# Kernel tuning notes

Measured on AMD Instinct MI355X. Metric: run time of the kernel, lower is better.

The kernel has to match this reference:

```python
import jax, jax.numpy as jnp
import numpy as np
import math

HEADS = 16
MAX_LEN = 512  # tokens; seq must equal this for the relative bias to be valid
D_HEAD = 64
BH = 256  # batch*heads


def setup_inputs() -> dict:
    key = jax.random.key(0)
    k1, k2, k3, k4 = jax.random.split(key, 4)
    S, B, D = MAX_LEN, BH, D_HEAD
    return {
        "query": jax.random.normal(k1, (S, B, D), dtype=jnp.float32),
        "key": jax.random.normal(k2, (S, B, D), dtype=jnp.float32),
        "value": jax.random.normal(k3, (S, B, D), dtype=jnp.float32),
        # per-head relative position embedding table [heads, 2*tokens-1, d_head]
        "k_rpos_emb": jax.random.normal(k4, (HEADS, 2 * MAX_LEN - 1, D), dtype=jnp.float32),
    }


def reference(query, key, value, k_rpos_emb):
    # 'seq b f -> b seq f'
    q = jnp.transpose(query, (1, 0, 2))   # [bh, s, d]
    k = jnp.transpose(key, (1, 0, 2))
    v = jnp.transpose(value, (1, 0, 2))
    bh, s, d = q.shape
    b = bh // HEADS

    # relative position bias from keys: split heads, contract with per-head table
    kh = k.reshape(b, HEADS, s, d)                                   # [b,h,s,d]
    rel_logits = jnp.einsum('bhid,hrd->bhir', kh, k_rpos_emb)        # [b,h,s,2L-1]
    rel_idx = (jnp.arange(s)[None, :] - jnp.arange(s)[:, None]
               + MAX_LEN - 1).astype(jnp.int32)                      # [s,s] in [0,2L-2]
    rel_bias = jnp.take_along_axis(
        rel_logits, rel_idx[None, None, :, :], axis=-1)              # [b,h,s,s]
    rel_bias = rel_bias.reshape(bh, s, s)

    scale = 1.0 / math.sqrt(d)
    scores = (jnp.einsum('bid,bjd->bij', q, k) + rel_bias) * scale   # [bh,s,s]
    attn = jax.nn.softmax(scores, axis=-1)
    out = jnp.einsum('bij,bjd->bid', attn, v)                        # [bh,s,d]
    return jnp.transpose(out, (1, 0, 2))                             # [s,bh,d]
```

## Files before the change

kernel.cpp:

```cpp
#include <hip/hip_runtime.h>
#include <hip/hip_bf16.h>

#define S_LEN  512
#define D_DIM  64
#define NH     16
#define R_LEN  1023
#define BHD    16384
#define PPITCH 68

typedef __attribute__((ext_vector_type(8))) short   short8_t;
typedef __attribute__((ext_vector_type(8))) __bf16  bf16x8;
typedef __attribute__((ext_vector_type(4))) float   floatx4;

__device__ __forceinline__ unsigned short f2bf(float f) {
  union { float f; unsigned u; } v; v.f = f;
  return (unsigned short)((v.u + 0x7fffu + ((v.u >> 16) & 1u)) >> 16);
}
__device__ __forceinline__ ushort2 c2(float x, float y) {
  __hip_bfloat162 h = __float22bfloat162_rn(float2{x, y});
  union { __hip_bfloat162 h; ushort2 u; } v; v.h = h; return v.u;
}
__device__ __forceinline__ short8_t pack8s(float4 a, float4 b) {
  union { ushort2 u2[4]; short8_t s8; } u;
  u.u2[0] = c2(a.x, a.y); u.u2[1] = c2(a.z, a.w);
  u.u2[2] = c2(b.x, b.y); u.u2[3] = c2(b.z, b.w);
  return u.s8;
}
__device__ __forceinline__ bf16x8 pack8(float4 a, float4 b) {
  short8_t s = pack8s(a, b);
  return __builtin_bit_cast(bf16x8, s);
}
__device__ __forceinline__ bf16x8 ldfrag(const unsigned short* p) {
  short8_t s = *(const short8_t*)p;
  return __builtin_bit_cast(bf16x8, s);
}
__device__ __forceinline__ bf16x8 ldfrag8(const unsigned short* p) {
  union { ushort4 u4[2]; short8_t s8; } u;
  u.u4[0] = *(const ushort4*)p;
  u.u4[1] = *(const ushort4*)(p + 4);
  return __builtin_bit_cast(bf16x8, u.s8);
}
__device__ __forceinline__ bf16x8 ldseg(const unsigned short* buf, int r, int seg) {
  return ldfrag(buf + r * 64 + ((seg ^ (r & 7)) << 3));
}
__device__ __forceinline__ void async16(const void* g, void* l) {
  __builtin_amdgcn_global_load_lds(
      (const __attribute__((address_space(1))) unsigned int*)(unsigned long long)(uintptr_t)g,
      (__attribute__((address_space(3))) unsigned int*)(unsigned int)(uintptr_t)l,
      16, 0, 0);
}
__device__ __forceinline__ void stage16(const unsigned short* gb, size_t rstride,
                                        unsigned short* lb, int lane) {
  int srow = lane >> 3;
  int sseg = (lane & 7) ^ srow;
  async16(gb + (size_t)srow * rstride + sseg * 8, lb);
  async16(gb + (size_t)(srow + 8) * rstride + sseg * 8, lb + 512);
}
__device__ __forceinline__ void stageE(const unsigned short* gb, int sigma,
                                       unsigned short* slot, int lane, int wv) {
  int srow = lane >> 3;
  int sseg = (lane & 7) ^ srow;
  int r0 = sigma * 64 + wv * 16 + srow;
  unsigned short* lb = slot + (wv * 16) * 64;
  async16(gb + (size_t)min(r0, R_LEN - 1) * D_DIM + sseg * 8, lb);
  async16(gb + (size_t)min(r0 + 8, R_LEN - 1) * D_DIM + sseg * 8, lb + 512);
}
template<int N>
__device__ __forceinline__ float dpp_ror(float x) {
  int i = __builtin_bit_cast(int, x);
  int r = __builtin_amdgcn_update_dpp(i, i, 0x120 + N, 0xF, 0xF, false);
  return __builtin_bit_cast(float, r);
}
__device__ __forceinline__ float rmax16(float x) {
  x = fmaxf(x, dpp_ror<8>(x)); x = fmaxf(x, dpp_ror<4>(x));
  x = fmaxf(x, dpp_ror<2>(x)); x = fmaxf(x, dpp_ror<1>(x));
  return x;
}
__device__ __forceinline__ float rsum16(float x) {
  x += dpp_ror<8>(x); x += dpp_ror<4>(x);
  x += dpp_ror<2>(x); x += dpp_ror<1>(x);
  return x;
}

extern "C" __global__ void prepass(const float* __restrict__ k, const float* __restrict__ v,
                                   const float* __restrict__ emb,
                                   unsigned short* __restrict__ kb,
                                   unsigned short* __restrict__ vtb,
                                   unsigned short* __restrict__ eb) {
  __shared__ unsigned short t[64 * PPITCH];
  const int bid = blockIdx.x;
  const int tid = threadIdx.x;
  if (bid < 4096) {
    size_t i = (size_t)bid * 256 + tid;
    const float* s = k + i * 8;
    float4 a = *(const float4*)s, b = *(const float4*)(s + 4);
    *(short8_t*)(kb + i * 8) = pack8s(a, b);
  } else if (bid < 4608) {
    size_t i = (size_t)(bid - 4096) * 256 + tid;
    if (i < 130944) {
      const float* s = emb + i * 8;
      float4 a = *(const float4*)s, b = *(const float4*)(s + 4);
      *(short8_t*)(eb + i * 8) = pack8s(a, b);
    }
  } else {
    const int b2 = bid - 4608;
    const int bh = b2 >> 3;
    const int j0 = (b2 & 7) << 6;
    for (int idx = tid; idx < 1024; idx += 256) {
      int jl = idx >> 4, cg = (idx & 15) << 2;
      float4 a = *(const float4*)(v + (size_t)(j0 + jl) * BHD + bh * D_DIM + cg);
      ushort2 u0 = c2(a.x, a.y), u1 = c2(a.z, a.w);
      *(ushort4*)(t + jl * PPITCH + cg) = (ushort4){ u0.x, u0.y, u1.x, u1.y };
    }
    __syncthreads();
    for (int slot = tid; slot < 512; slot += 256) {
      int d = slot >> 3, jseg = slot & 7;
      union { unsigned short u[8]; short8_t s8; } r;
      #pragma unroll
      for (int jj = 0; jj < 8; ++jj) r.u[jj] = t[(jseg * 8 + jj) * PPITCH + d];
      *(short8_t*)(vtb + ((size_t)bh * D_DIM + d) * S_LEN + j0 + jseg * 8) = r.s8;
    }
  }
}

extern "C" __global__ __launch_bounds__(256, 2)
void attn_relbias(const float* __restrict__ q, const unsigned short* __restrict__ kb,
                  const unsigned short* __restrict__ vtb,
                  const unsigned short* __restrict__ eb,
                  float* __restrict__ out)
{
  __shared__ unsigned short kbuf[2][4096];
  __shared__ unsigned short vbuf[2][4096];
  __shared__ unsigned short ebuf[3][4096];
  __shared__ unsigned short ps[4][16 * PPITCH];

  const int tid  = threadIdx.x;
  const int bh   = blockIdx.x & 255;
  const int i0   = (blockIdx.x >> 8) << 6;
  const int h    = bh & (NH - 1);
  const int wv   = tid >> 6;
  const int lane = tid & 63;
  const int l15  = lane & 15;
  const int quad = lane >> 4;
  const int iloc0 = wv * 16 + quad * 4;
  const int elo   = 3 - wv;
  const int arow  = wv * 16 + l15;
  const int acol  = quad * 8;
  const int it0   = 7 - (i0 >> 6);

  const unsigned short* kgb  = kb  + (size_t)bh * D_DIM;
  const unsigned short* vgb  = vtb + (size_t)bh * (D_DIM * S_LEN);
  const unsigned short* egb  = eb  + (size_t)h * (R_LEN * D_DIM);

  stage16(kgb + (size_t)(wv * 16) * BHD, BHD, &kbuf[0][(wv * 16) * 64], lane);
  stage16(vgb + (size_t)(wv * 16) * S_LEN, S_LEN, &vbuf[0][(wv * 16) * 64], lane);
  stageE(egb, it0,     ebuf[it0 % 3],       lane, wv);
  stageE(egb, it0 + 1, ebuf[(it0 + 1) % 3], lane, wv);

  bf16x8 qa0, qa1, ia0, ia1;
  {
    const float* gq = q + (size_t)(i0 + arow) * BHD + bh * D_DIM + acol;
    qa0 = pack8(*(const float4*)gq,        *(const float4*)(gq + 4));
    qa1 = pack8(*(const float4*)(gq + 32), *(const float4*)(gq + 36));
    const unsigned short* gi = kb + (size_t)(i0 + arow) * BHD + bh * D_DIM + acol;
    ia0 = ldfrag(gi);
    ia1 = ldfrag(gi + 32);
  }

  floatx4 oacc[4];
  #pragma unroll
  for (int c = 0; c < 4; ++c) oacc[c] = (floatx4){0.f, 0.f, 0.f, 0.f};
  float m_i[4] = { -1e30f, -1e30f, -1e30f, -1e30f };
  float l_i[4] = { 0.f, 0.f, 0.f, 0.f };

  __syncthreads();

  #pragma unroll 2
  for (int t = 0; t < 8; ++t) {
    if (t < 7) {
      const int j1 = t * 64 + 64;
      stage16(kgb + (size_t)(j1 + wv * 16) * BHD, BHD, &kbuf[(t + 1) & 1][(wv * 16) * 64], lane);
      stage16(vgb + (size_t)(wv * 16) * S_LEN + j1, S_LEN, &vbuf[(t + 1) & 1][(wv * 16) * 64], lane);
      stageE(egb, it0 + t + 2, ebuf[(it0 + t + 2) % 3], lane, wv);
    }
    const unsigned short* kc = kbuf[t & 1];
    const unsigned short* vc = vbuf[t & 1];

    floatx4 bacc[5];
    #pragma unroll
    for (int ei = 0; ei < 5; ++ei) {
      const int eblk = elo + ei;
      const unsigned short* es = ebuf[(it0 + t + (eblk >> 2)) % 3];
      const int lr = (eblk * 16 + l15) & 63;
      floatx4 bz = (floatx4){0.f, 0.f, 0.f, 0.f};
      bz = __builtin_amdgcn_mfma_f32_16x16x32_bf16(ia0, ldseg(es, lr, quad),     bz, 0, 0, 0);
      bz = __builtin_amdgcn_mfma_f32_16x16x32_bf16(ia1, ldseg(es, lr, quad + 4), bz, 0, 0, 0);
      bacc[ei] = bz;
    }

    floatx4 qk[4];
    #pragma unroll
    for (int c = 0; c < 4; ++c) {
      floatx4 acc = (floatx4){0.f, 0.f, 0.f, 0.f};
      acc = __builtin_amdgcn_mfma_f32_16x16x32_bf16(qa0, ldseg(kc, c * 16 + l15, quad),     acc, 0, 0, 0);
      acc = __builtin_amdgcn_mfma_f32_16x16x32_bf16(qa1, ldseg(kc, c * 16 + l15, quad + 4), acc, 0, 0, 0);
      qk[c] = acc;
    }

    float sc[4][4];
    #pragma unroll
    for (int r = 0; r < 4; ++r) {
      const int o  = 15 - 4 * quad - r;
      const int ls = (lane & 48) + ((l15 + o) & 15);
      const bool hi = (l15 + o) >= 16;
      #pragma unroll
      for (int c = 0; c < 4; ++c) {
        float blo = __shfl(bacc[c][r],     ls);
        float bhi = __shfl(bacc[c + 1][r], ls);
        sc[c][r] = (qk[c][r] + (hi ? bhi : blo)) * 0.125f;
      }
    }

    float p[4][4];
    #pragma unroll
    for (int r = 0; r < 4; ++r) {
      float mx = fmaxf(fmaxf(sc[0][r], sc[1][r]), fmaxf(sc[2][r], sc[3][r]));
      mx = rmax16(mx);
      float mnew  = fmaxf(m_i[r], mx);
      float alpha = __expf(m_i[r] - mnew);
      float rs = 0.f;
      #pragma unroll
      for (int c = 0; c < 4; ++c) { p[c][r] = __expf(sc[c][r] - mnew); rs += p[c][r]; }
      rs = rsum16(rs);
      l_i[r] = l_i[r] * alpha + rs;
      m_i[r] = mnew;
      #pragma unroll
      for (int c = 0; c < 4; ++c) oacc[c][r] *= alpha;
    }

    unsigned short* psw = ps[wv];
    #pragma unroll
    for (int r = 0; r < 4; ++r) {
      ushort2 u01 = c2(p[0][r], p[1][r]);
      ushort2 u23 = c2(p[2][r], p[3][r]);
      unsigned short* pr = psw + (quad * 4 + r) * PPITCH + l15;
      pr[0]  = u01.x; pr[16] = u01.y; pr[32] = u23.x; pr[48] = u23.y;
    }
    bf16x8 pa0 = ldfrag8(psw + l15 * PPITCH + acol);
    bf16x8 pa1 = ldfrag8(psw + l15 * PPITCH + acol + 32);

    #pragma unroll
    for (int c = 0; c < 4; ++c) {
      oacc[c] = __builtin_amdgcn_mfma_f32_16x16x32_bf16(pa0, ldseg(vc, c * 16 + l15, quad),     oacc[c], 0, 0, 0);
      oacc[c] = __builtin_amdgcn_mfma_f32_16x16x32_bf16(pa1, ldseg(vc, c * 16 + l15, quad + 4), oacc[c], 0, 0, 0);
    }

    __syncthreads();
  }

  #pragma unroll
  for (int r = 0; r < 4; ++r) {
    float inv = 1.f / l_i[r];
    int row = i0 + iloc0 + r;
    #pragma unroll
    for (int c = 0; c < 4; ++c)
      out[(size_t)row * BHD + bh * D_DIM + c * 16 + l15] = oacc[c][r] * inv;
  }
}

#define PITCH 72
extern "C" __global__ __launch_bounds__(256, 4)
void attn_fb(const float* __restrict__ q, const float* __restrict__ k,
             const float* __restrict__ v, const float* __restrict__ emb,
             float* __restrict__ out)
{
  __shared__ unsigned short kjs[64 * PITCH];
  __shared__ unsigned short vts[64 * PITCH];
  __shared__ unsigned short ps2[4][16 * PPITCH];

  const int tid  = threadIdx.x;
  const int bh   = blockIdx.x >> 3;
  const int i0   = (blockIdx.x & 7) << 6;
  const int h    = bh & (NH - 1);
  const int wv   = tid >> 6;
  const int lane = tid & 63;
  const int l15  = lane & 15;
  const int quad = lane >> 4;
  const int iloc0 = wv * 16 + quad * 4;
  const int elo   = 3 - wv;

  {
    const float* gq = q + (size_t)i0 * BHD + bh * D_DIM;
    const float* gk = k + (size_t)i0 * BHD + bh * D_DIM;
    for (int idx = tid; idx < 1024; idx += 256) {
      int row = idx >> 4, cg = (idx & 15) << 2;
      float4 a = *(const float4*)(gq + row * BHD + cg);
      float4 b = *(const float4*)(gk + row * BHD + cg);
      *(ushort4*)(vts + row * PITCH + cg) = (ushort4){ f2bf(a.x), f2bf(a.y), f2bf(a.z), f2bf(a.w) };
      *(ushort4*)(kjs + row * PITCH + cg) = (ushort4){ f2bf(b.x), f2bf(b.y), f2bf(b.z), f2bf(b.w) };
    }
  }
  __syncthreads();

  const int arow = wv * 16 + l15;
  const int acol = quad * 8;
  bf16x8 qa0 = ldfrag(vts + arow * PITCH + acol);
  bf16x8 qa1 = ldfrag(vts + arow * PITCH + acol + 32);
  bf16x8 ia0 = ldfrag(kjs + arow * PITCH + acol);
  bf16x8 ia1 = ldfrag(kjs + arow * PITCH + acol + 32);

  floatx4 oacc[4];
  #pragma unroll
  for (int c = 0; c < 4; ++c) oacc[c] = (floatx4){0.f, 0.f, 0.f, 0.f};
  float m_i[4] = { -1e30f, -1e30f, -1e30f, -1e30f };
  float l_i[4] = { 0.f, 0.f, 0.f, 0.f };

  for (int j0 = 0; j0 < S_LEN; j0 += 64) {
    __syncthreads();
    {
      const float* gk = k + (size_t)j0 * BHD + bh * D_DIM;
      for (int idx = tid; idx < 1024; idx += 256) {
        int row = idx >> 4, cg = (idx & 15) << 2;
        float4 b = *(const float4*)(gk + row * BHD + cg);
        *(ushort4*)(kjs + row * PITCH + cg) = (ushort4){ f2bf(b.x), f2bf(b.y), f2bf(b.z), f2bf(b.w) };
      }
    }
    {
      const float* gv = v + (size_t)j0 * BHD + bh * D_DIM;
      for (int idx = tid; idx < 1024; idx += 256) {
        int dg = idx & 15, jl = idx >> 4;
        float4 b = *(const float4*)(gv + jl * BHD + dg * 4);
        int d0 = dg * 4;
        vts[(d0 + 0) * PITCH + jl] = f2bf(b.x);
        vts[(d0 + 1) * PITCH + jl] = f2bf(b.y);
        vts[(d0 + 2) * PITCH + jl] = f2bf(b.z);
        vts[(d0 + 3) * PITCH + jl] = f2bf(b.w);
      }
    }
    floatx4 bacc[5];
    {
      const int rbase = j0 - i0 + 448;
      #pragma unroll
      for (int ei = 0; ei < 5; ++ei) {
        int rg = rbase + (elo + ei) * 16 + l15;
        rg = min(rg, R_LEN - 1);
        const float* ep = emb + ((size_t)h * R_LEN + rg) * D_DIM + acol;
        float4 e0 = *(const float4*)(ep);
        float4 e1 = *(const float4*)(ep + 4);
        float4 e2 = *(const float4*)(ep + 32);
        float4 e3 = *(const float4*)(ep + 36);
        floatx4 bz = (floatx4){0.f, 0.f, 0.f, 0.f};
        bz = __builtin_amdgcn_mfma_f32_16x16x32_bf16(ia0, pack8(e0, e1), bz, 0, 0, 0);
        bz = __builtin_amdgcn_mfma_f32_16x16x32_bf16(ia1, pack8(e2, e3), bz, 0, 0, 0);
        bacc[ei] = bz;
      }
    }
    __syncthreads();

    floatx4 qk[4];
    #pragma unroll
    for (int c = 0; c < 4; ++c) {
      bf16x8 kb0 = ldfrag(kjs + (c * 16 + l15) * PITCH + acol);
      bf16x8 kb1 = ldfrag(kjs + (c * 16 + l15) * PITCH + acol + 32);
      floatx4 acc = (floatx4){0.f, 0.f, 0.f, 0.f};
      acc = __builtin_amdgcn_mfma_f32_16x16x32_bf16(qa0, kb0, acc, 0, 0, 0);
      acc = __builtin_amdgcn_mfma_f32_16x16x32_bf16(qa1, kb1, acc, 0, 0, 0);
      qk[c] = acc;
    }
    float sc[4][4];
    #pragma unroll
    for (int r = 0; r < 4; ++r) {
      const int o  = 15 - 4 * quad - r;
      const int ls = (lane & 48) + ((l15 + o) & 15);
      const bool hi = (l15 + o) >= 16;
      #pragma unroll
      for (int c = 0; c < 4; ++c) {
        float blo = __shfl(bacc[c][r],     ls);
        float bhi = __shfl(bacc[c + 1][r], ls);
        sc[c][r] = (qk[c][r] + (hi ? bhi : blo)) * 0.125f;
      }
    }
    float p[4][4];
    #pragma unroll
    for (int r = 0; r < 4; ++r) {
      float mx = fmaxf(fmaxf(sc[0][r], sc[1][r]), fmaxf(sc[2][r], sc[3][r]));
      mx = rmax16(mx);
      float mnew  = fmaxf(m_i[r], mx);
      float alpha = __expf(m_i[r] - mnew);
      float rs = 0.f;
      #pragma unroll
      for (int c = 0; c < 4; ++c) { p[c][r] = __expf(sc[c][r] - mnew); rs += p[c][r]; }
      rs = rsum16(rs);
      l_i[r] = l_i[r] * alpha + rs;
      m_i[r] = mnew;
      #pragma unroll
      for (int c = 0; c < 4; ++c) oacc[c][r] *= alpha;
    }
    unsigned short* psw = ps2[wv];
    #pragma unroll
    for (int c = 0; c < 4; ++c) {
      #pragma unroll
      for (int r = 0; r < 4; ++r)
        psw[(quad * 4 + r) * PPITCH + c * 16 + l15] = f2bf(p[c][r]);
    }
    bf16x8 pa0 = ldfrag8(psw + l15 * PPITCH + acol);
    bf16x8 pa1 = ldfrag8(psw + l15 * PPITCH + acol + 32);
    #pragma unroll
    for (int c = 0; c < 4; ++c) {
      bf16x8 vb0 = ldfrag(vts + (c * 16 + l15) * PITCH + acol);
      bf16x8 vb1 = ldfrag(vts + (c * 16 + l15) * PITCH + acol + 32);
      oacc[c] = __builtin_amdgcn_mfma_f32_16x16x32_bf16(pa0, vb0, oacc[c], 0, 0, 0);
      oacc[c] = __builtin_amdgcn_mfma_f32_16x16x32_bf16(pa1, vb1, oacc[c], 0, 0, 0);
    }
  }
  #pragma unroll
  for (int r = 0; r < 4; ++r) {
    float inv = 1.f / l_i[r];
    int row = i0 + iloc0 + r;
    #pragma unroll
    for (int c = 0; c < 4; ++c)
      out[(size_t)row * BHD + bh * D_DIM + c * 16 + l15] = oacc[c][r] * inv;
  }
}

extern "C" void kernel_launch(void* const* d_in, const int* in_sizes, int n_in,
                              void* d_out, int out_size, void* d_ws, size_t ws_size,
                              hipStream_t stream) {
  const float* q   = (const float*)d_in[0];
  const float* k   = (const float*)d_in[1];
  const float* v   = (const float*)d_in[2];
  const float* emb = (const float*)d_in[3];
  float* out = (float*)d_out;

  const size_t kb_off  = 0;
  const size_t vtb_off = (size_t)512 * 256 * 64 * 2;
  const size_t eb_off  = vtb_off * 2;
  const size_t need    = eb_off + (size_t)NH * R_LEN * D_DIM * 2;

  if (ws_size >= need) {
    unsigned short* kbp  = (unsigned short*)((char*)d_ws + kb_off);
    unsigned short* vtbp = (unsigned short*)((char*)d_ws + vtb_off);
    unsigned short* ebp  = (unsigned short*)((char*)d_ws + eb_off);
    hipLaunchKernelGGL(prepass, dim3(6656), dim3(256), 0, stream, k, v, emb, kbp, vtbp, ebp);
    hipLaunchKernelGGL(attn_relbias, dim3(2048), dim3(256), 0, stream,
                       q, kbp, vtbp, ebp, out);
  } else {
    hipLaunchKernelGGL(attn_fb, dim3(2048), dim3(256), 0, stream, q, k, v, emb, out);
  }
}
```

Measured before the change: 214.0 us.

## Load relative-embedding fragments directly from global, drop E LDS ring, raise occupancy

Removes the triple-buffered LDS staging of the per-head relative position embedding table. Each lane now loads its E fragments directly from global/L2 into registers, with the loads split around the QK MFMAs to hide latency. The P scratch buffer is repacked to a 64-wide XOR-swizzled layout so it fits without padding. Together with the smaller LDS footprint, launch bounds are raised from 2 to 4 blocks per CU for higher occupancy. The trade-off is more global load traffic and register pressure for the E fragments, and the register cap implied by 4 blocks/CU could cause spills.

```diff
diff --git a/kernel.cpp b/kernel.cpp
--- a/kernel.cpp
+++ b/kernel.cpp
@@ -7,6 +7,7 @@
 #define R_LEN  1023
 #define BHD    16384
 #define PPITCH 68
+#define EMAXB  130816
 
 typedef __attribute__((ext_vector_type(8))) short   short8_t;
 typedef __attribute__((ext_vector_type(8))) __bf16  bf16x8;
@@ -55,15 +56,6 @@
   int sseg = (lane & 7) ^ srow;
   async16(gb + (size_t)srow * rstride + sseg * 8, lb);
   async16(gb + (size_t)(srow + 8) * rstride + sseg * 8, lb + 512);
-}
-__device__ __forceinline__ void stageE(const unsigned short* gb, int sigma,
-                                       unsigned short* slot, int lane, int wv) {
-  int srow = lane >> 3;
-  int sseg = (lane & 7) ^ srow;
-  int r0 = sigma * 64 + wv * 16 + srow;
-  unsigned short* lb = slot + (wv * 16) * 64;
-  async16(gb + (size_t)min(r0, R_LEN - 1) * D_DIM + sseg * 8, lb);
-  async16(gb + (size_t)min(r0 + 8, R_LEN - 1) * D_DIM + sseg * 8, lb + 512);
 }
 template<int N>
 __device__ __forceinline__ float dpp_ror(float x) {
@@ -123,7 +115,7 @@
   }
 }
 
-extern "C" __global__ __launch_bounds__(256, 2)
+extern "C" __global__ __launch_bounds__(256, 4)
 void attn_relbias(const float* __restrict__ q, const unsigned short* __restrict__ kb,
                   const unsigned short* __restrict__ vtb,
                   const unsigned short* __restrict__ eb,
@@ -131,8 +123,7 @@
 {
   __shared__ unsigned short kbuf[2][4096];
   __shared__ unsigned short vbuf[2][4096];
-  __shared__ unsigned short ebuf[3][4096];
-  __shared__ unsigned short ps[4][16 * PPITCH];
+  __shared__ unsigned short ps[4][16 * 64];
 
   const int tid  = threadIdx.x;
   const int bh   = blockIdx.x & 255;
@@ -150,12 +141,15 @@
 
   const unsigned short* kgb  = kb  + (size_t)bh * D_DIM;
   const unsigned short* vgb  = vtb + (size_t)bh * (D_DIM * S_LEN);
-  const unsigned short* egb  = eb  + (size_t)h * (R_LEN * D_DIM);
+
+  const char* egB = (const char*)(eb + (size_t)h * (R_LEN * D_DIM)) + (quad << 4);
+  int eoff[5];
+  #pragma unroll
+  for (int ei = 0; ei < 5; ++ei)
+    eoff[ei] = (it0 * 64 + (elo + ei) * 16 + l15) * 128;
 
   stage16(kgb + (size_t)(wv * 16) * BHD, BHD, &kbuf[0][(wv * 16) * 64], lane);
   stage16(vgb + (size_t)(wv * 16) * S_LEN, S_LEN, &vbuf[0][(wv * 16) * 64], lane);
-  stageE(egb, it0,     ebuf[it0 % 3],       lane, wv);
-  stageE(egb, it0 + 1, ebuf[(it0 + 1) % 3], lane, wv);
 
   bf16x8 qa0, qa1, ia0, ia1;
   {
@@ -181,21 +175,16 @@
       const int j1 = t * 64 + 64;
       stage16(kgb + (size_t)(j1 + wv * 16) * BHD, BHD, &kbuf[(t + 1) & 1][(wv * 16) * 64], lane);
       stage16(vgb + (size_t)(wv * 16) * S_LEN + j1, S_LEN, &vbuf[(t + 1) & 1][(wv * 16) * 64], lane);
-      stageE(egb, it0 + t + 2, ebuf[(it0 + t + 2) % 3], lane, wv);
     }
     const unsigned short* kc = kbuf[t & 1];
     const unsigned short* vc = vbuf[t & 1];
 
-    floatx4 bacc[5];
-    #pragma unroll
-    for (int ei = 0; ei < 5; ++ei) {
-      const int eblk = elo + ei;
-      const unsigned short* es = ebuf[(it0 + t + (eblk >> 2)) % 3];
-      const int lr = (eblk * 16 + l15) & 63;
-      floatx4 bz = (floatx4){0.f, 0.f, 0.f, 0.f};
-      bz = __builtin_amdgcn_mfma_f32_16x16x32_bf16(ia0, ldseg(es, lr, quad),     bz, 0, 0, 0);
-      bz = __builtin_amdgcn_mfma_f32_16x16x32_bf16(ia1, ldseg(es, lr, quad + 4), bz, 0, 0, 0);
-      bacc[ei] = bz;
+    bf16x8 ef0[5], ef1[5];
+    #pragma unroll
+    for (int ei = 0; ei < 3; ++ei) {
+      int bo = min(eoff[ei], EMAXB);
+      ef0[ei] = ldfrag((const unsigned short*)(egB + bo));
+      ef1[ei] = ldfrag((const unsigned short*)(egB + bo + 64));
     }
 
     floatx4 qk[4];
@@ -206,6 +195,22 @@
       acc = __builtin_amdgcn_mfma_f32_16x16x32_bf16(qa1, ldseg(kc, c * 16 + l15, quad + 4), acc, 0, 0, 0);
       qk[c] = acc;
     }
+
+    floatx4 bacc[5];
+    #pragma unroll
+    for (int ei = 0; ei < 5; ++ei) {
+      if (ei < 2) {
+        int bo = min(eoff[ei + 3], EMAXB);
+        ef0[ei + 3] = ldfrag((const unsigned short*)(egB + bo));
+        ef1[ei + 3] = ldfrag((const unsigned short*)(egB + bo + 64));
+      }
+      floatx4 bz = (floatx4){0.f, 0.f, 0.f, 0.f};
+      bz = __builtin_amdgcn_mfma_f32_16x16x32_bf16(ia0, ef0[ei], bz, 0, 0, 0);
+      bz = __builtin_amdgcn_mfma_f32_16x16x32_bf16(ia1, ef1[ei], bz, 0, 0, 0);
+      bacc[ei] = bz;
+    }
+    #pragma unroll
+    for (int ei = 0; ei < 5; ++ei) eoff[ei] += 8192;
 
     float sc[4][4];
     #pragma unroll
@@ -243,11 +248,14 @@
     for (int r = 0; r < 4; ++r) {
       ushort2 u01 = c2(p[0][r], p[1][r]);
       ushort2 u23 = c2(p[2][r], p[3][r]);
-      unsigned short* pr = psw + (quad * 4 + r) * PPITCH + l15;
-      pr[0]  = u01.x; pr[16] = u01.y; pr[32] = u23.x; pr[48] = u23.y;
-    }
-    bf16x8 pa0 = ldfrag8(psw + l15 * PPITCH + acol);
-    bf16x8 pa1 = ldfrag8(psw + l15 * PPITCH + acol + 32);
+      unsigned short* pr = psw + (quad * 4 + r) * 64 + l15;
+      pr[(0 ^ quad) << 4] = u01.x; pr[(1 ^ quad) << 4] = u01.y;
+      pr[(2 ^ quad) << 4] = u23.x; pr[(3 ^ quad) << 4] = u23.y;
+    }
+    const int g = l15 >> 2;
+    const unsigned short* prd = psw + l15 * 64 + ((quad & 1) << 3);
+    bf16x8 pa0 = ldfrag(prd + ((((quad >> 1)    ) ^ g) << 4));
+    bf16x8 pa1 = ldfrag(prd + ((((quad >> 1) + 2) ^ g) << 4));
 
     #pragma unroll
     for (int c = 0; c < 4; ++c) {
```

Result: slower. 224.6 us (+5.0%).

## Process two 64-row query subtiles per block to reuse K/V tiles

Applied to the files above, without the earlier changes.

Each attention block now covers 128 query rows as two 64-row subtiles, so every staged K, V and relative-embedding tile serves both subtiles, and the grid is halved. The K and V fragments loaded from shared memory are reused across both subtiles' MFMAs. The embedding ring grows to four buffers to cover the extra diagonal block. Softmax also switches to exp2 with the log2e factor folded into the score scale. The cost is twice the accumulator and score registers per thread, which risks spills under the two-blocks-per-SM launch bound, and fewer blocks in the grid.

```diff
diff --git a/kernel.cpp b/kernel.cpp
--- a/kernel.cpp
+++ b/kernel.cpp
@@ -7,6 +7,7 @@
 #define R_LEN  1023
 #define BHD    16384
 #define PPITCH 68
+#define SCL2   0.1803368801111204f
 
 typedef __attribute__((ext_vector_type(8))) short   short8_t;
 typedef __attribute__((ext_vector_type(8))) __bf16  bf16x8;
@@ -80,6 +81,13 @@
   x += dpp_ror<8>(x); x += dpp_ror<4>(x);
   x += dpp_ror<2>(x); x += dpp_ror<1>(x);
   return x;
+}
+__device__ __forceinline__ float fexp2(float x) {
+#if __has_builtin(__builtin_amdgcn_exp2f)
+  return __builtin_amdgcn_exp2f(x);
+#else
+  return exp2f(x);
+#endif
 }
 
 extern "C" __global__ void prepass(const float* __restrict__ k, const float* __restrict__ v,
@@ -131,12 +139,12 @@
 {
   __shared__ unsigned short kbuf[2][4096];
   __shared__ unsigned short vbuf[2][4096];
-  __shared__ unsigned short ebuf[3][4096];
+  __shared__ unsigned short ebuf[4][4096];
   __shared__ unsigned short ps[4][16 * PPITCH];
 
   const int tid  = threadIdx.x;
   const int bh   = blockIdx.x & 255;
-  const int i0   = (blockIdx.x >> 8) << 6;
+  const int i0   = (blockIdx.x >> 8) << 7;
   const int h    = bh & (NH - 1);
   const int wv   = tid >> 6;
   const int lane = tid & 63;
@@ -154,24 +162,32 @@
 
   stage16(kgb + (size_t)(wv * 16) * BHD, BHD, &kbuf[0][(wv * 16) * 64], lane);
   stage16(vgb + (size_t)(wv * 16) * S_LEN, S_LEN, &vbuf[0][(wv * 16) * 64], lane);
-  stageE(egb, it0,     ebuf[it0 % 3],       lane, wv);
-  stageE(egb, it0 + 1, ebuf[(it0 + 1) % 3], lane, wv);
-
-  bf16x8 qa0, qa1, ia0, ia1;
-  {
-    const float* gq = q + (size_t)(i0 + arow) * BHD + bh * D_DIM + acol;
-    qa0 = pack8(*(const float4*)gq,        *(const float4*)(gq + 4));
-    qa1 = pack8(*(const float4*)(gq + 32), *(const float4*)(gq + 36));
-    const unsigned short* gi = kb + (size_t)(i0 + arow) * BHD + bh * D_DIM + acol;
-    ia0 = ldfrag(gi);
-    ia1 = ldfrag(gi + 32);
-  }
-
-  floatx4 oacc[4];
+  stageE(egb, it0 - 1, ebuf[(it0 - 1) & 3], lane, wv);
+  stageE(egb, it0,     ebuf[it0 & 3],       lane, wv);
+  stageE(egb, it0 + 1, ebuf[(it0 + 1) & 3], lane, wv);
+
+  bf16x8 qa0[2], qa1[2], ia0[2], ia1[2];
   #pragma unroll
-  for (int c = 0; c < 4; ++c) oacc[c] = (floatx4){0.f, 0.f, 0.f, 0.f};
-  float m_i[4] = { -1e30f, -1e30f, -1e30f, -1e30f };
-  float l_i[4] = { 0.f, 0.f, 0.f, 0.f };
+  for (int st = 0; st < 2; ++st) {
+    const int row = i0 + st * 64 + arow;
+    const float* gq = q + (size_t)row * BHD + bh * D_DIM + acol;
+    qa0[st] = pack8(*(const float4*)gq,        *(const float4*)(gq + 4));
+    qa1[st] = pack8(*(const float4*)(gq + 32), *(const float4*)(gq + 36));
+    const unsigned short* gi = kb + (size_t)row * BHD + bh * D_DIM + acol;
+    ia0[st] = ldfrag(gi);
+    ia1[st] = ldfrag(gi + 32);
+  }
+
+  floatx4 oacc[2][4];
+  float m_i[2][4], l_i[2][4];
+  #pragma unroll
+  for (int st = 0; st < 2; ++st) {
+    #pragma unroll
+    for (int r = 0; r < 4; ++r) {
+      oacc[st][r] = (floatx4){0.f, 0.f, 0.f, 0.f};
+      m_i[st][r] = -1e30f; l_i[st][r] = 0.f;
+    }
+  }
 
   __syncthreads();
 
@@ -181,90 +197,124 @@
       const int j1 = t * 64 + 64;
       stage16(kgb + (size_t)(j1 + wv * 16) * BHD, BHD, &kbuf[(t + 1) & 1][(wv * 16) * 64], lane);
       stage16(vgb + (size_t)(wv * 16) * S_LEN + j1, S_LEN, &vbuf[(t + 1) & 1][(wv * 16) * 64], lane);
-      stageE(egb, it0 + t + 2, ebuf[(it0 + t + 2) % 3], lane, wv);
+      stageE(egb, it0 + t + 2, ebuf[(it0 + t + 2) & 3], lane, wv);
     }
     const unsigned short* kc = kbuf[t & 1];
     const unsigned short* vc = vbuf[t & 1];
 
-    floatx4 bacc[5];
-    #pragma unroll
-    for (int ei = 0; ei < 5; ++ei) {
-      const int eblk = elo + ei;
-      const unsigned short* es = ebuf[(it0 + t + (eblk >> 2)) % 3];
-      const int lr = (eblk * 16 + l15) & 63;
-      floatx4 bz = (floatx4){0.f, 0.f, 0.f, 0.f};
-      bz = __builtin_amdgcn_mfma_f32_16x16x32_bf16(ia0, ldseg(es, lr, quad),     bz, 0, 0, 0);
-      bz = __builtin_amdgcn_mfma_f32_16x16x32_bf16(ia1, ldseg(es, lr, quad + 4), bz, 0, 0, 0);
-      bacc[ei] = bz;
-    }
-
-    floatx4 qk[4];
+    floatx4 bacc[2][5];
+    #pragma unroll
+    for (int st = 0; st < 2; ++st) {
+      const int sbase = it0 - st + t;
+      #pragma unroll
+      for (int ei = 0; ei < 5; ++ei) {
+        const int eblk = elo + ei;
+        const unsigned short* es = ebuf[(sbase + (eblk >> 2)) & 3];
+        const int lr = (eblk * 16 + l15) & 63;
+        floatx4 bz = (floatx4){0.f, 0.f, 0.f, 0.f};
+        bz = __builtin_amdgcn_mfma_f32_16x16x32_bf16(ia0[st], ldseg(es, lr, quad),     bz, 0, 0, 0);
+        bz = __builtin_amdgcn_mfma_f32_16x16x32_bf16(ia1[st], ldseg(es, lr, quad + 4), bz, 0, 0, 0);
+        bacc[st][ei] = bz;
+      }
+    }
+
+    floatx4 qk[2][4];
     #pragma unroll
     for (int c = 0; c < 4; ++c) {
-      floatx4 acc = (floatx4){0.f, 0.f, 0.f, 0.f};
-      acc = __builtin_amdgcn_mfma_f32_16x16x32_bf16(qa0, ldseg(kc, c * 16 + l15, quad),     acc, 0, 0, 0);
-      acc = __builtin_amdgcn_mfma_f32_16x16x32_bf16(qa1, ldseg(kc, c * 16 + l15, quad + 4), acc, 0, 0, 0);
-      qk[c] = acc;
-    }
-
-    float sc[4][4];
+      bf16x8 k0 = ldseg(kc, c * 16 + l15, quad);
+      bf16x8 k1 = ldseg(kc, c * 16 + l15, quad + 4);
+      #pragma unroll
+      for (int st = 0; st < 2; ++st) {
+        floatx4 acc = (floatx4){0.f, 0.f, 0.f, 0.f};
+        acc = __builtin_amdgcn_mfma_f32_16x16x32_bf16(qa0[st], k0, acc, 0, 0, 0);
+        acc = __builtin_amdgcn_mfma_f32_16x16x32_bf16(qa1[st], k1, acc, 0, 0, 0);
+        qk[st][c] = acc;
+      }
+    }
+
+    float p[2][4][4];
+    #pragma unroll
+    for (int st = 0; st < 2; ++st) {
+      float sc[4][4];
+      #pragma unroll
+      for (int r = 0; r < 4; ++r) {
+        const int o  = 15 - 4 * quad - r;
+        const int ls = (lane & 48) + ((l15 + o) & 15);
+        const bool hi = (l15 + o) >= 16;
+        #pragma unroll
+        for (int c = 0; c < 4; ++c) {
+          float blo = __shfl(bacc[st][c][r],     ls);
+          float bhi = __shfl(bacc[st][c + 1][r], ls);
+          sc[c][r] = (qk[st][c][r] + (hi ? bhi : blo)) * SCL2;
+        }
+      }
+      #pragma unroll
+      for (int r = 0; r < 4; ++r) {
+        float mx = fmaxf(fmaxf(sc[0][r], sc[1][r]), fmaxf(sc[2][r], sc[3][r]));
+        mx = rmax16(mx);
+        float mnew  = fmaxf(m_i[st][r], mx);
+        float alpha = fexp2(m_i[st][r] - mnew);
+        float rs = 0.f;
+        #pragma unroll
+        for (int c = 0; c < 4; ++c) { p[st][c][r] = fexp2(sc[c][r] - mnew); rs += p[st][c][r]; }
+        rs = rsum16(rs);
+        l_i[st][r] = l_i[st][r] * alpha + rs;
+        m_i[st][r] = mnew;
+        #pragma unroll
+        for (int c = 0; c < 4; ++c) oacc[st][c][r] *= alpha;
+      }
+    }
+
+    unsigned short* psw = ps[wv];
+    bf16x8 vb0[4], vb1[4];
+    {
+      #pragma unroll
+      for (int r = 0; r < 4; ++r) {
+        ushort2 u01 = c2(p[0][0][r], p[0][1][r]);
+        ushort2 u23 = c2(p[0][2][r], p[0][3][r]);
+        unsigned short* pr = psw + (quad * 4 + r) * PPITCH + l15;
+        pr[0]  = u01.x; pr[16] = u01.y; pr[32] = u23.x; pr[48] = u23.y;
+      }
+      bf16x8 pa0 = ldfrag8(psw + l15 * PPITCH + acol);
+      bf16x8 pa1 = ldfrag8(psw + l15 * PPITCH + acol + 32);
+      #pragma unroll
+      for (int c = 0; c < 4; ++c) {
+        vb0[c] = ldseg(vc, c * 16 + l15, quad);
+        vb1[c] = ldseg(vc, c * 16 + l15, quad + 4);
+        oacc[0][c] = __builtin_amdgcn_mfma_f32_16x16x32_bf16(pa0, vb0[c], oacc[0][c], 0, 0, 0);
+        oacc[0][c] = __builtin_amdgcn_mfma_f32_16x16x32_bf16(pa1, vb1[c], oacc[0][c], 0, 0, 0);
+      }
+    }
+    {
+      #pragma unroll
+      for (int r = 0; r < 4; ++r) {
+        ushort2 u01 = c2(p[1][0][r], p[1][1][r]);
+        ushort2 u23 = c2(p[1][2][r], p[1][3][r]);
+        unsigned short* pr = psw + (quad * 4 + r) * PPITCH + l15;
+        pr[0]  = u01.x; pr[16] = u01.y; pr[32] = u23.x; pr[48] = u23.y;
+      }
+      bf16x8 pa0 = ldfrag8(psw + l15 * PPITCH + acol);
+      bf16x8 pa1 = ldfrag8(psw + l15 * PPITCH + acol + 32);
+      #pragma unroll
+      for (int c = 0; c < 4; ++c) {
+        oacc[1][c] = __builtin_amdgcn_mfma_f32_16x16x32_bf16(pa0, vb0[c], oacc[1][c], 0, 0, 0);
+        oacc[1][c] = __builtin_amdgcn_mfma_f32_16x16x32_bf16(pa1, vb1[c], oacc[1][c], 0, 0, 0);
+      }
+    }
+
+    __syncthreads();
+  }
+
+  #pragma unroll
+  for (int st = 0; st < 2; ++st) {
     #pragma unroll
     for (int r = 0; r < 4; ++r) {
-      const int o  = 15 - 4 * quad - r;
-      const int ls = (lane & 48) + ((l15 + o) & 15);
-      const bool hi = (l15 + o) >= 16;
-      #pragma unroll
-      for (int c = 0; c < 4; ++c) {
-        float blo = __shfl(bacc[c][r],     ls);
-        float bhi = __shfl(bacc[c + 1][r], ls);
-        sc[c][r] = (qk[c][r] + (hi ? bhi : blo)) * 0.125f;
-      }
-    }
-
-    float p[4][4];
-    #pragma unroll
-    for (int r = 0; r < 4; ++r) {
-      float mx = fmaxf(fmaxf(sc[0][r], sc[1][r]), fmaxf(sc[2][r], sc[3][r]));
-      mx = rmax16(mx);
-      float mnew  = fmaxf(m_i[r], mx);
-      float alpha = __expf(m_i[r] - mnew);
-      float rs = 0.f;
-      #pragma unroll
-      for (int c = 0; c < 4; ++c) { p[c][r] = __expf(sc[c][r] - mnew); rs += p[c][r]; }
-      rs = rsum16(rs);
-      l_i[r] = l_i[r] * alpha + rs;
-      m_i[r] = mnew;
-      #pragma unroll
-      for (int c = 0; c < 4; ++c) oacc[c][r] *= alpha;
-    }
-
-    unsigned short* psw = ps[wv];
-    #pragma unroll
-    for (int r = 0; r < 4; ++r) {
-      ushort2 u01 = c2(p[0][r], p[1][r]);
-      ushort2 u23 = c2(p[2][r], p[3][r]);
-      unsigned short* pr = psw + (quad * 4 + r) * PPITCH + l15;
-      pr[0]  = u01.x; pr[16] = u01.y; pr[32] = u23.x; pr[48] = u23.y;
-    }
-    bf16x8 pa0 = ldfrag8(psw + l15 * PPITCH + acol);
-    bf16x8 pa1 = ldfrag8(psw + l15 * PPITCH + acol + 32);
-
-    #pragma unroll
-    for (int c = 0; c < 4; ++c) {
-      oacc[c] = __builtin_amdgcn_mfma_f32_16x16x32_bf16(pa0, ldseg(vc, c * 16 + l15, quad),     oacc[c], 0, 0, 0);
-      oacc[c] = __builtin_amdgcn_mfma_f32_16x16x32_bf16(pa1, ldseg(vc, c * 16 + l15, quad + 4), oacc[c], 0, 0, 0);
-    }
-
-    __syncthreads();
-  }
-
-  #pragma unroll
-  for (int r = 0; r < 4; ++r) {
-    float inv = 1.f / l_i[r];
-    int row = i0 + iloc0 + r;
-    #pragma unroll
-    for (int c = 0; c < 4; ++c)
-      out[(size_t)row * BHD + bh * D_DIM + c * 16 + l15] = oacc[c][r] * inv;
+      float inv = 1.f / l_i[st][r];
+      int row = i0 + st * 64 + iloc0 + r;
+      #pragma unroll
+      for (int c = 0; c < 4; ++c)
+        out[(size_t)row * BHD + bh * D_DIM + c * 16 + l15] = oacc[st][c][r] * inv;
+    }
   }
 }
 
@@ -442,7 +492,7 @@
     unsigned short* vtbp = (unsigned short*)((char*)d_ws + vtb_off);
     unsigned short* ebp  = (unsigned short*)((char*)d_ws + eb_off);
     hipLaunchKernelGGL(prepass, dim3(6656), dim3(256), 0, stream, k, v, emb, kbp, vtbp, ebp);
-    hipLaunchKernelGGL(attn_relbias, dim3(2048), dim3(256), 0, stream,
+    hipLaunchKernelGGL(attn_relbias, dim3(1024), dim3(256), 0, stream,
                        q, kbp, vtbp, ebp, out);
   } else {
     hipLaunchKernelGGL(attn_fb, dim3(2048), dim3(256), 0, stream, q, k, v, emb, out);
```

Result: faster. 201.5 us (-5.8%).
